# Performance work log

Hardware: AMD Instinct MI355X
Metric: run time of the kernel (lower is better)

Reference implementation:

```python
import jax, jax.numpy as jnp
import numpy as np
from jax import lax

EPS = 1e-5

def setup_inputs() -> dict:
    key = jax.random.key(0)
    k1, k2 = jax.random.split(key)
    x = jax.random.normal(k1, (32, 256, 56, 56), dtype=jnp.float32)
    W = jax.random.normal(k2, (256, 256, 3, 3), dtype=jnp.float32) * 0.05  # real-valued latent weights
    gamma = jnp.ones((256,), dtype=jnp.float32)
    beta = jnp.zeros((256,), dtype=jnp.float32)
    return {"x": x, "W": W, "gamma": gamma, "beta": beta}

def reference(x, W, gamma, beta):
    # Binarize weights to {-1,+1} (deterministic sign, as in BinaryConnect)
    Wb = jnp.sign(W)
    # Conv: stride 1, padding 1, NCHW/OIHW -> [B, 256, 56, 56]
    y = lax.conv_general_dilated(x, Wb, window_strides=(1, 1),
                                 padding=[(1, 1), (1, 1)],
                                 dimension_numbers=("NCHW", "OIHW", "NCHW"))
    # BatchNorm2d (training mode: batch statistics, biased variance)
    mean = jnp.mean(y, axis=(0, 2, 3), keepdims=True)
    var = jnp.mean((y - mean) ** 2, axis=(0, 2, 3), keepdims=True)
    y = (y - mean) * lax.rsqrt(var + EPS)
    y = y * gamma[None, :, None, None] + beta[None, :, None, None]
    # ReLU
    y = jnp.maximum(y, 0.0)
    # MaxPool2d kernel 2, stride 2 -> [B, 256, 28, 28]
    y = lax.reduce_window(y, -jnp.inf, lax.max,
                          window_dimensions=(1, 1, 2, 2),
                          window_strides=(1, 1, 2, 2),
                          padding="VALID")
    return y
```

## Files before the change

### kernel.cpp

```cpp
#include <hip/hip_runtime.h>
#include <stdint.h>

typedef int i32x4  __attribute__((ext_vector_type(4)));
typedef int i32x16 __attribute__((ext_vector_type(16)));

#define M_TOTAL   100352
#define PLANE_I8  1722368L
#define WQ_OFF    27557888L
#define Y_OFF     28147712L
#define STATS_OFF 79527936L
#define QS   21.166666f
#define SYQ  0.047244094f
#define SC16 0.755905509f

__global__ void prep_w(const float* __restrict__ W, char* __restrict__ wq) {
  int idx = blockIdx.x * 256 + threadIdx.x;
  int e  = idx & 15;
  int co = (idx >> 4) & 255;
  int ck = idx >> 12;
  int f  = ck >> 4;
  int ci = ((ck & 15) << 4) | e;
  int kh = (f * 11) >> 5;
  int kw = f - kh * 3;
  float v = W[((co * 256 + ci) * 3 + kh) * 3 + kw];
  wq[idx] = v < 0.0f ? (char)-1 : (char)1;
}

__global__ void border_zero(char* __restrict__ xq) {
  int idx = blockIdx.x * 256 + threadIdx.x;
  int g = idx & 15;
  int p = (idx >> 4) % 228;
  int n = (idx >> 4) / 228;
  int h, w;
  if (p < 58)       { h = 0;  w = p; }
  else if (p < 116) { h = 57; w = p - 58; }
  else { int q = p - 116; h = 1 + (q >> 1); w = 57 * (q & 1); }
  long r = ((long)n * 58 + h) * 58 + w;
  *(uint4*)(xq + g * PLANE_I8 + r * 16) = make_uint4(0, 0, 0, 0);
}

__global__ void prep_x(const float* __restrict__ x, char* __restrict__ xq) {
  int b = blockIdx.x;
  int cblk = b & 3;
  int nh = b >> 2;
  int hp = nh % 28, n = nh / 28;
  __shared__ float tile[64][114];
  int tid = threadIdx.x;
  const float* src = x + (((long)n * 256 + cblk * 64) * 56 + hp * 2) * 56;
#pragma unroll
  for (int i = 0; i < 7; ++i) {
    int idx = i * 256 + tid;
    int cl = idx / 28, rem = idx - cl * 28;
    int h2 = rem / 14, v4 = rem - h2 * 14;
    float4 d = *(const float4*)(src + (long)cl * 3136 + h2 * 56 + v4 * 4);
    float* tp = &tile[cl][h2 * 57 + v4 * 4];
    tp[0] = d.x; tp[1] = d.y; tp[2] = d.z; tp[3] = d.w;
  }
  __syncthreads();
  char* base = xq + (long)(cblk * 4) * PLANE_I8
               + (((long)n * 58 + hp * 2 + 1) * 58 + 1) * 16;
#pragma unroll
  for (int i = 0; i < 2; ++i) {
    int idx = i * 256 + tid;
    if (idx < 448) {
      int g4 = idx & 3, h2 = (idx >> 2) & 1, wq_ = idx >> 3;
      union { uint4 u; char c[16]; } d;
#pragma unroll
      for (int e = 0; e < 16; ++e) {
        int q = __float2int_rn(tile[g4 * 16 + e][h2 * 57 + wq_] * QS);
        q = q > 127 ? 127 : (q < -127 ? -127 : q);
        d.c[e] = (char)q;
      }
      *(uint4*)(base + (long)g4 * PLANE_I8 + (h2 * 58 + wq_) * 16) = d.u;
    }
  }
}

__global__ __launch_bounds__(256, 3) void conv_gemm(
    const char* __restrict__ xq, const char* __restrict__ wq,
    short* __restrict__ y16, float* __restrict__ stats) {
  const int tid = threadIdx.x;
  const int w = tid >> 6, l = tid & 63;
  const int gm = blockIdx.x >> 1;
  const int gn = blockIdx.x & 1;
  const int wm = w >> 1, wn = w & 1;
  const int l31 = l & 31, lh = l >> 5;

  long voffA0, voffA1;
  {
    long vs[2];
#pragma unroll
    for (int rb = 0; rb < 2; ++rb) {
      int gr = gm * 128 + wm * 64 + rb * 32 + l31;
      int n = gr / 3136, rem = gr - n * 3136;
      int hh = rem / 56, wx = rem - hh * 56;
      vs[rb] = (long)lh * PLANE_I8 + (((long)n * 58 + hh) * 58 + wx) * 16;
    }
    voffA0 = vs[0]; voffA1 = vs[1];
  }
  const long voffB = (long)lh * 4096 + (gn * 128 + wn * 64 + l31) * 16;

  i32x4 a0[2][2], a1[2][2], a2[2][2];
  i32x4 b0[2][2], b1[2][2], b2[2][2];
  i32x16 acc[2][2] = {};

#define LOADA(F, CS, DST)                                                    \
  {                                                                          \
    const int kh_ = ((F) * 11) >> 5;                                         \
    const int kw_ = (F) - kh_ * 3;                                           \
    const char* ba = xq + (long)(CS) * 4 * PLANE_I8 + (kh_ * 58 + kw_) * 16; \
    DST[0][0] = *(const i32x4*)(ba + voffA0);                                \
    DST[0][1] = *(const i32x4*)(ba + voffA1);                                \
    const char* ba1 = ba + 2 * PLANE_I8;                                     \
    DST[1][0] = *(const i32x4*)(ba1 + voffA0);                               \
    DST[1][1] = *(const i32x4*)(ba1 + voffA1);                               \
  }
#define LOADB(F, CS, DST)                                                    \
  {                                                                          \
    const char* bb = wq + (long)(((F) << 4) + ((CS) << 2)) * 4096 + voffB;   \
    DST[0][0] = *(const i32x4*)(bb);                                         \
    DST[0][1] = *(const i32x4*)(bb + 512);                                   \
    DST[1][0] = *(const i32x4*)(bb + 8192);                                  \
    DST[1][1] = *(const i32x4*)(bb + 8192 + 512);                            \
  }
#define MFMA8(A, B)                                                          \
  {                                                                          \
    _Pragma("unroll")                                                        \
    for (int kc = 0; kc < 2; ++kc)                                           \
      _Pragma("unroll")                                                      \
      for (int rb = 0; rb < 2; ++rb) {                                       \
        acc[rb][0] = __builtin_amdgcn_mfma_i32_32x32x32_i8(                  \
            A[kc][rb], B[kc][0], acc[rb][0], 0, 0, 0);                       \
        acc[rb][1] = __builtin_amdgcn_mfma_i32_32x32x32_i8(                  \
            A[kc][rb], B[kc][1], acc[rb][1], 0, 0, 0);                       \
      }                                                                      \
  }

  LOADA(0, 0, a0); LOADB(0, 0, b0);
  LOADA(1, 0, a1); LOADB(1, 0, b1);
  LOADA(2, 0, a2); LOADB(2, 0, b2);
  int f0 = 3, cs0 = 0, f1 = 4, cs1 = 0, f2 = 5, cs2 = 0;

  for (int i = 0; i < 12; ++i) {
    MFMA8(a0, b0);
    if (i < 11) {
      LOADA(f0, cs0, a0); LOADB(f0, cs0, b0);
      f0 += 3; if (f0 >= 9) { f0 -= 9; ++cs0; }
    }
    MFMA8(a1, b1);
    if (i < 11) {
      LOADA(f1, cs1, a1); LOADB(f1, cs1, b1);
      f1 += 3; if (f1 >= 9) { f1 -= 9; ++cs1; }
    }
    MFMA8(a2, b2);
    if (i < 11) {
      LOADA(f2, cs2, a2); LOADB(f2, cs2, b2);
      f2 += 3; if (f2 >= 9) { f2 -= 9; ++cs2; }
    }
  }
#undef LOADA
#undef LOADB
#undef MFMA8

#pragma unroll
  for (int cb = 0; cb < 2; ++cb) {
    float s = 0.f, q = 0.f;
#pragma unroll
    for (int rb = 0; rb < 2; ++rb)
#pragma unroll
      for (int j = 0; j < 16; ++j) {
        float v = SYQ * (float)acc[rb][cb][j];
        s += v; q += v * v;
      }
    s += __shfl_xor(s, 32, 64);
    q += __shfl_xor(q, 32, 64);
    if (lh == 0) {
      int col = gn * 128 + wn * 64 + cb * 32 + l31;
      atomicAdd(&stats[col], s);
      atomicAdd(&stats[256 + col], q);
    }
  }

  const long rbase = (long)gm * 128 + wm * 64;
  const int  cbase = gn * 128 + wn * 64 + l31;
#pragma unroll
  for (int rb = 0; rb < 2; ++rb)
#pragma unroll
    for (int j = 0; j < 16; ++j) {
      long rr = rbase + rb * 32 + (j & 3) + 8 * (j >> 2) + 4 * lh;
      short* dst = y16 + rr * 256 + cbase;
      dst[0]  = (short)((acc[rb][0][j] + 8) >> 4);
      dst[32] = (short)((acc[rb][1][j] + 8) >> 4);
    }
}

__global__ void bn_stats(const float* __restrict__ stats, const float* __restrict__ gamma,
                         const float* __restrict__ beta, float* __restrict__ sc) {
  int c = threadIdx.x;
  const float inv = 1.0f / (float)M_TOTAL;
  float mean = stats[c] * inv;
  float var  = stats[256 + c] * inv - mean * mean;
  float s = gamma[c] * rsqrtf(var + 1e-5f);
  sc[c] = s * SC16;
  sc[256 + c] = beta[c] - mean * s;
}

__global__ void bn_pool(const short* __restrict__ y16, const float* __restrict__ sc,
                        float* __restrict__ out) {
  int b = blockIdx.x;
  int ho = b % 28, n = b / 28;
  __shared__ short t[256][113];
  __shared__ float ssc[256], ssb[256];
  int tid = threadIdx.x;
  ssc[tid] = sc[tid];
  ssb[tid] = sc[256 + tid];
  const short* src = y16 + (((long)n * 56 + ho * 2) * 56) * 256;
#pragma unroll
  for (int i = 0; i < 14; ++i) {
    int v = i * 256 + tid;
    int cv = v & 31, hw = v >> 5;
    union { uint4 u; short h[8]; } d;
    d.u = *(const uint4*)(src + (long)hw * 256 + cv * 8);
#pragma unroll
    for (int e = 0; e < 8; ++e) t[cv * 8 + e][hw] = d.h[e];
  }
  __syncthreads();
  float* dst = out + (long)n * 200704 + ho * 28;
#pragma unroll
  for (int i = 0; i < 7; ++i) {
    int oidx = i * 256 + tid;
    int co = oidx / 7, wq4 = oidx - co * 7;
    float s = ssc[co], bb = ssb[co];
    int w0 = wq4 * 8;
    float4 o;
    {
      float r0 = fmaf(s, (float)t[co][w0 + 0], bb), r1 = fmaf(s, (float)t[co][w0 + 1], bb);
      float r2 = fmaf(s, (float)t[co][56 + w0 + 0], bb), r3 = fmaf(s, (float)t[co][56 + w0 + 1], bb);
      o.x = fmaxf(fmaxf(fmaxf(r0, r1), fmaxf(r2, r3)), 0.f);
    }
    {
      float r0 = fmaf(s, (float)t[co][w0 + 2], bb), r1 = fmaf(s, (float)t[co][w0 + 3], bb);
      float r2 = fmaf(s, (float)t[co][56 + w0 + 2], bb), r3 = fmaf(s, (float)t[co][56 + w0 + 3], bb);
      o.y = fmaxf(fmaxf(fmaxf(r0, r1), fmaxf(r2, r3)), 0.f);
    }
    {
      float r0 = fmaf(s, (float)t[co][w0 + 4], bb), r1 = fmaf(s, (float)t[co][w0 + 5], bb);
      float r2 = fmaf(s, (float)t[co][56 + w0 + 4], bb), r3 = fmaf(s, (float)t[co][56 + w0 + 5], bb);
      o.z = fmaxf(fmaxf(fmaxf(r0, r1), fmaxf(r2, r3)), 0.f);
    }
    {
      float r0 = fmaf(s, (float)t[co][w0 + 6], bb), r1 = fmaf(s, (float)t[co][w0 + 7], bb);
      float r2 = fmaf(s, (float)t[co][56 + w0 + 6], bb), r3 = fmaf(s, (float)t[co][56 + w0 + 7], bb);
      o.w = fmaxf(fmaxf(fmaxf(r0, r1), fmaxf(r2, r3)), 0.f);
    }
    *(float4*)(dst + (long)co * 784 + wq4 * 4) = o;
  }
}

extern "C" void kernel_launch(void* const* d_in, const int* in_sizes, int n_in,
                              void* d_out, int out_size, void* d_ws, size_t ws_size,
                              hipStream_t stream) {
  const float* x     = (const float*)d_in[0];
  const float* W     = (const float*)d_in[1];
  const float* gamma = (const float*)d_in[2];
  const float* beta  = (const float*)d_in[3];
  float* out = (float*)d_out;
  char* ws = (char*)d_ws;
  char*  xq    = ws;
  char*  wq    = ws + WQ_OFF;
  short* y16   = (short*)(ws + Y_OFF);
  float* stats = (float*)(ws + STATS_OFF);

  hipMemsetAsync(stats, 0, 512 * sizeof(float), stream);
  hipLaunchKernelGGL(border_zero, dim3(456), dim3(256), 0, stream, xq);
  hipLaunchKernelGGL(prep_w, dim3(2304), dim3(256), 0, stream, W, wq);
  hipLaunchKernelGGL(prep_x, dim3(32 * 28 * 4), dim3(256), 0, stream, x, xq);
  hipLaunchKernelGGL(conv_gemm, dim3(1568), dim3(256), 0, stream, xq, wq, y16, stats);
  hipLaunchKernelGGL(bn_stats, dim3(1), dim3(256), 0, stream, stats, gamma, beta, stats + 512);
  hipLaunchKernelGGL(bn_pool, dim3(32 * 28), dim3(256), 0, stream, y16, stats + 512, out);
}
```

Baseline: 139.5 us.

## Stage conv GEMM operands through LDS with direct global-to-LDS double buffering

Replaces per-wave direct register loads of A and B fragments with cooperative global_load_lds transfers into double-buffered shared memory. Each operand element is then fetched from global once per block instead of redundantly per wave, and MFMA blocks are bracketed by setprio. The trade-off is two barriers per k-step and a shallower prefetch depth than the previous triple-buffered register pipeline, which can expose memory latency.

```diff
diff --git a/kernel.cpp b/kernel.cpp
--- a/kernel.cpp
+++ b/kernel.cpp
@@ -3,6 +3,9 @@
 
 typedef int i32x4  __attribute__((ext_vector_type(4)));
 typedef int i32x16 __attribute__((ext_vector_type(16)));
+
+typedef const __attribute__((address_space(1))) void* gptr_t;
+typedef __attribute__((address_space(3))) void* sptr_t;
 
 #define M_TOTAL   100352
 #define PLANE_I8  1722368L
@@ -12,6 +15,10 @@
 #define QS   21.166666f
 #define SYQ  0.047244094f
 #define SC16 0.755905509f
+
+__device__ __forceinline__ void gload_lds16(const void* g, void* l) {
+  __builtin_amdgcn_global_load_lds((gptr_t)g, (sptr_t)l, 16, 0, 0);
+}
 
 __global__ void prep_w(const float* __restrict__ W, char* __restrict__ wq) {
   int idx = blockIdx.x * 256 + threadIdx.x;
@@ -79,6 +86,9 @@
 __global__ __launch_bounds__(256, 3) void conv_gemm(
     const char* __restrict__ xq, const char* __restrict__ wq,
     short* __restrict__ y16, float* __restrict__ stats) {
+  __shared__ __align__(16) char As[2][4][128][16];
+  __shared__ __align__(16) char Bs[2][4][128][16];
+
   const int tid = threadIdx.x;
   const int w = tid >> 6, l = tid & 63;
   const int gm = blockIdx.x >> 1;
@@ -86,81 +96,75 @@
   const int wm = w >> 1, wn = w & 1;
   const int l31 = l & 31, lh = l >> 5;
 
-  long voffA0, voffA1;
+  long rowoffA;
   {
-    long vs[2];
-#pragma unroll
-    for (int rb = 0; rb < 2; ++rb) {
-      int gr = gm * 128 + wm * 64 + rb * 32 + l31;
-      int n = gr / 3136, rem = gr - n * 3136;
-      int hh = rem / 56, wx = rem - hh * 56;
-      vs[rb] = (long)lh * PLANE_I8 + (((long)n * 58 + hh) * 58 + wx) * 16;
-    }
-    voffA0 = vs[0]; voffA1 = vs[1];
-  }
-  const long voffB = (long)lh * 4096 + (gn * 128 + wn * 64 + l31) * 16;
-
-  i32x4 a0[2][2], a1[2][2], a2[2][2];
-  i32x4 b0[2][2], b1[2][2], b2[2][2];
+    int gr = gm * 128 + ((w & 1) << 6) + l;
+    int n = gr / 3136, rem = gr - n * 3136;
+    int hh = rem / 56, wx = rem - hh * 56;
+    rowoffA = (((long)n * 58 + hh) * 58 + wx) * 16;
+  }
+  const int ksw = w >> 1;
+  const long coloffB = (long)(gn * 128 + ((w & 1) << 6) + l) * 16;
+  char* ldsA0 = &As[0][0][0][0] + w * 1024;
+  char* ldsB0 = &Bs[0][0][0][0] + w * 1024;
+
+  auto stage = [&](int buf, int f, int cs) {
+    const int kh = (f * 11) >> 5;
+    const int kw = f - kh * 3;
+    const char* gaJ0 = xq + (long)(cs * 4 + ksw) * PLANE_I8
+                       + (kh * 58 + kw) * 16 + rowoffA;
+    const char* gbJ0 = wq + (long)(f * 16 + cs * 4 + ksw) * 4096 + coloffB;
+    char* la = ldsA0 + buf * 8192;
+    char* lb = ldsB0 + buf * 8192;
+    gload_lds16(gaJ0,                  la);
+    gload_lds16(gaJ0 + 2 * PLANE_I8,   la + 4096);
+    gload_lds16(gbJ0,                  lb);
+    gload_lds16(gbJ0 + 2 * 4096,       lb + 4096);
+  };
+
   i32x16 acc[2][2] = {};
 
-#define LOADA(F, CS, DST)                                                    \
-  {                                                                          \
-    const int kh_ = ((F) * 11) >> 5;                                         \
-    const int kw_ = (F) - kh_ * 3;                                           \
-    const char* ba = xq + (long)(CS) * 4 * PLANE_I8 + (kh_ * 58 + kw_) * 16; \
-    DST[0][0] = *(const i32x4*)(ba + voffA0);                                \
-    DST[0][1] = *(const i32x4*)(ba + voffA1);                                \
-    const char* ba1 = ba + 2 * PLANE_I8;                                     \
-    DST[1][0] = *(const i32x4*)(ba1 + voffA0);                               \
-    DST[1][1] = *(const i32x4*)(ba1 + voffA1);                               \
-  }
-#define LOADB(F, CS, DST)                                                    \
-  {                                                                          \
-    const char* bb = wq + (long)(((F) << 4) + ((CS) << 2)) * 4096 + voffB;   \
-    DST[0][0] = *(const i32x4*)(bb);                                         \
-    DST[0][1] = *(const i32x4*)(bb + 512);                                   \
-    DST[1][0] = *(const i32x4*)(bb + 8192);                                  \
-    DST[1][1] = *(const i32x4*)(bb + 8192 + 512);                            \
-  }
-#define MFMA8(A, B)                                                          \
-  {                                                                          \
-    _Pragma("unroll")                                                        \
-    for (int kc = 0; kc < 2; ++kc)                                           \
-      _Pragma("unroll")                                                      \
-      for (int rb = 0; rb < 2; ++rb) {                                       \
-        acc[rb][0] = __builtin_amdgcn_mfma_i32_32x32x32_i8(                  \
-            A[kc][rb], B[kc][0], acc[rb][0], 0, 0, 0);                       \
-        acc[rb][1] = __builtin_amdgcn_mfma_i32_32x32x32_i8(                  \
-            A[kc][rb], B[kc][1], acc[rb][1], 0, 0, 0);                       \
-      }                                                                      \
-  }
-
-  LOADA(0, 0, a0); LOADB(0, 0, b0);
-  LOADA(1, 0, a1); LOADB(1, 0, b1);
-  LOADA(2, 0, a2); LOADB(2, 0, b2);
-  int f0 = 3, cs0 = 0, f1 = 4, cs1 = 0, f2 = 5, cs2 = 0;
-
-  for (int i = 0; i < 12; ++i) {
-    MFMA8(a0, b0);
-    if (i < 11) {
-      LOADA(f0, cs0, a0); LOADB(f0, cs0, b0);
-      f0 += 3; if (f0 >= 9) { f0 -= 9; ++cs0; }
-    }
-    MFMA8(a1, b1);
-    if (i < 11) {
-      LOADA(f1, cs1, a1); LOADB(f1, cs1, b1);
-      f1 += 3; if (f1 >= 9) { f1 -= 9; ++cs1; }
-    }
-    MFMA8(a2, b2);
-    if (i < 11) {
-      LOADA(f2, cs2, a2); LOADB(f2, cs2, b2);
-      f2 += 3; if (f2 >= 9) { f2 -= 9; ++cs2; }
-    }
-  }
-#undef LOADA
-#undef LOADB
-#undef MFMA8
+  stage(0, 0, 0);
+  int fS = 1, csS = 0;
+
+  int buf = 0;
+  for (int t = 0; t < 36; ++t) {
+    if (t + 1 < 36) {
+      stage(buf ^ 1, fS, csS);
+      ++fS; if (fS == 9) { fS = 0; ++csS; }
+      asm volatile("s_waitcnt vmcnt(4)" ::: "memory");
+    } else {
+      asm volatile("s_waitcnt vmcnt(0)" ::: "memory");
+    }
+    __builtin_amdgcn_s_barrier();
+    asm volatile("" ::: "memory");
+
+    i32x4 av[2][2], bv[2][2];
+#pragma unroll
+    for (int kc = 0; kc < 2; ++kc) {
+#pragma unroll
+      for (int rb = 0; rb < 2; ++rb)
+        av[kc][rb] = *(const i32x4*)&As[buf][kc * 2 + lh][wm * 64 + rb * 32 + l31][0];
+#pragma unroll
+      for (int cb = 0; cb < 2; ++cb)
+        bv[kc][cb] = *(const i32x4*)&Bs[buf][kc * 2 + lh][wn * 64 + cb * 32 + l31][0];
+    }
+    __builtin_amdgcn_s_setprio(1);
+#pragma unroll
+    for (int kc = 0; kc < 2; ++kc)
+#pragma unroll
+      for (int rb = 0; rb < 2; ++rb) {
+        acc[rb][0] = __builtin_amdgcn_mfma_i32_32x32x32_i8(
+            av[kc][rb], bv[kc][0], acc[rb][0], 0, 0, 0);
+        acc[rb][1] = __builtin_amdgcn_mfma_i32_32x32x32_i8(
+            av[kc][rb], bv[kc][1], acc[rb][1], 0, 0, 0);
+      }
+    __builtin_amdgcn_s_setprio(0);
+    asm volatile("s_waitcnt lgkmcnt(0)" ::: "memory");
+    __builtin_amdgcn_s_barrier();
+    asm volatile("" ::: "memory");
+    buf ^= 1;
+  }
 
 #pragma unroll
   for (int cb = 0; cb < 2; ++cb) {
```

Result: slower. 149.0 us (+6.8%).
